# Kernel tuning notes

Hardware: AMD Instinct MI355X
Metric: run time of the kernel (lower is better)

The kernel has to match this reference:

```python
import jax, jax.numpy as jnp
import numpy as np

SEQ, BATCH, IN, HID = 512, 64, 512, 1024


def setup_inputs() -> dict:
    key = jax.random.key(0)
    k_x, k_wih, k_whh, k_bih, k_bhh = jax.random.split(key, 5)
    s = 1.0 / np.sqrt(HID)  # PyTorch GRU init: U(-1/sqrt(H), 1/sqrt(H))
    return {
        "x": jax.random.normal(k_x, (SEQ, BATCH, IN), dtype=jnp.float32),
        "W_ih": jax.random.uniform(k_wih, (3 * HID, IN), jnp.float32, -s, s),
        "W_hh": jax.random.uniform(k_whh, (3 * HID, HID), jnp.float32, -s, s),
        "b_ih": jax.random.uniform(k_bih, (3 * HID,), jnp.float32, -s, s),
        "b_hh": jax.random.uniform(k_bhh, (3 * HID,), jnp.float32, -s, s),
    }


def reference(x, W_ih, W_hh, b_ih, b_hh):
    """Single-layer GRU, PyTorch gate semantics, h0 = 0.
    r = sig(Wir x + bir + Whr h + bhr); z = sig(...);
    n = tanh(Win x + bin + r * (Whn h + bhn)); h' = (1-z)*n + z*h.
    Returns (outputs [S,B,H], hidden [1,B,H])."""
    H = W_hh.shape[1]
    # Precompute all input-side gate projections in one big GEMM: (S,B,3H)
    gates_x = jnp.einsum("sbi,gi->sbg", x, W_ih) + b_ih

    def step(h, gx):
        gh = h @ W_hh.T + b_hh  # (B, 3H)
        xr, xz, xn = jnp.split(gx, 3, axis=-1)
        hr, hz, hn = jnp.split(gh, 3, axis=-1)
        r = jax.nn.sigmoid(xr + hr)
        z = jax.nn.sigmoid(xz + hz)
        n = jnp.tanh(xn + r * hn)
        h_new = (1.0 - z) * n + z * h
        return h_new, h_new

    h0 = jnp.zeros((x.shape[1], H), dtype=x.dtype)
    h_last, ys = jax.lax.scan(step, h0, gates_x)
    return ys, h_last[None]  # match nn.GRU: (output, hidden[num_layers=1])
```

## Files before the change

kernel.cpp:

```cpp
#include <hip/hip_runtime.h>
#include <stdint.h>


#define SEQ    512
#define BATCH  64
#define IN_DIM 512
#define HID    1024
#define G3     3072
#define NBLK   256

typedef __bf16 bf16x8 __attribute__((ext_vector_type(8)));
typedef short  s16x8  __attribute__((ext_vector_type(8)));
typedef float  f32x4  __attribute__((ext_vector_type(4)));
typedef unsigned int u32x4 __attribute__((ext_vector_type(4)));

__device__ __forceinline__ float bf2f(unsigned int u) {
    union { unsigned int i; float f; } c; c.i = u << 16; return c.f;
}
__device__ __forceinline__ unsigned short f2bf(float f) {
    union { float f; unsigned int i; } c; c.f = f;
    unsigned int u = c.i;
    u += 0x7fffu + ((u >> 16) & 1u);
    return (unsigned short)(u >> 16);
}

__global__ void cvt_f32_bf16(const float* __restrict__ in,
                             unsigned short* __restrict__ out, int n) {
    int i = (blockIdx.x * 256 + threadIdx.x) * 4;
    if (i + 3 < n) {
        float4 v = *(const float4*)(in + i);
        ushort4 o;
        o.x = f2bf(v.x); o.y = f2bf(v.y); o.z = f2bf(v.z); o.w = f2bf(v.w);
        *(ushort4*)(out + i) = o;
    }
}

__global__ void init_state(unsigned int* __restrict__ h0,
                           unsigned int* __restrict__ h1,
                           unsigned int* __restrict__ flags) {
    int i = blockIdx.x * 256 + threadIdx.x;
    if (i < BATCH * HID) { h0[i] = 0u; h1[i] = 0u; }
    if (i < NBLK * 4)    flags[i] = 0u;
}

__global__ __launch_bounds__(256) void gx_gemm(
    const unsigned short* __restrict__ xb,
    const unsigned short* __restrict__ wb,
    const float* __restrict__ bih,
    unsigned short* __restrict__ gx) {
    const int lane = threadIdx.x & 63;
    const int wv   = threadIdx.x >> 6;
    const int r    = lane & 15;
    const int quad = lane >> 4;
    const int m0 = blockIdx.x * 128 + (wv & 1) * 64;
    const int n0 = blockIdx.y * 128 + (wv >> 1) * 64;

    f32x4 acc[4][4];
#pragma unroll
    for (int a = 0; a < 4; a++)
#pragma unroll
        for (int b = 0; b < 4; b++) acc[a][b] = (f32x4){0.f, 0.f, 0.f, 0.f};

    const unsigned short* ap[4];
    const unsigned short* bp[4];
#pragma unroll
    for (int mi = 0; mi < 4; mi++)
        ap[mi] = xb + (size_t)(m0 + mi * 16 + r) * IN_DIM + quad * 8;
#pragma unroll
    for (int ni = 0; ni < 4; ni++)
        bp[ni] = wb + (size_t)(n0 + ni * 16 + r) * IN_DIM + quad * 8;

#pragma unroll 4
    for (int kk = 0; kk < IN_DIM / 32; kk++) {
        bf16x8 af[4], bf_[4];
#pragma unroll
        for (int mi = 0; mi < 4; mi++)
            af[mi] = __builtin_bit_cast(bf16x8, *(const s16x8*)(ap[mi] + kk * 32));
#pragma unroll
        for (int ni = 0; ni < 4; ni++)
            bf_[ni] = __builtin_bit_cast(bf16x8, *(const s16x8*)(bp[ni] + kk * 32));
#pragma unroll
        for (int mi = 0; mi < 4; mi++)
#pragma unroll
            for (int ni = 0; ni < 4; ni++)
                acc[mi][ni] = __builtin_amdgcn_mfma_f32_16x16x32_bf16(
                    af[mi], bf_[ni], acc[mi][ni], 0, 0, 0);
    }

#pragma unroll
    for (int ni = 0; ni < 4; ni++) {
        const int col = n0 + ni * 16 + r;
        const float bias = bih[col];
#pragma unroll
        for (int mi = 0; mi < 4; mi++)
#pragma unroll
            for (int i = 0; i < 4; i++) {
                const int row = m0 + mi * 16 + quad * 4 + i;
                gx[(size_t)row * G3 + col] = f2bf(acc[mi][ni][i] + bias);
            }
    }
}

#define HL16(dst, OFF)                                                    \
    asm volatile("global_load_dwordx4 %0, %1, off offset:" OFF " sc0 sc1" \
                 : "=&v"(dst) : "v"(hbase))
#define SL4(dst, BASE)                                                    \
    asm volatile("global_load_dword %0, %1, off sc0 sc1"                  \
                 : "=&v"(dst) : "v"(BASE))

__global__ __launch_bounds__(256, 2) void gru_seq(
    const unsigned short* __restrict__ whb,
    const float* __restrict__ bhh,
    const unsigned short* __restrict__ gxb,
    unsigned int* __restrict__ h0,
    unsigned int* __restrict__ h1,
    unsigned int* __restrict__ flags,
    float* __restrict__ out) {
    const int lane = threadIdx.x & 63;
    const int wv   = threadIdx.x >> 6;
    const int r    = lane & 15;
    const int quad = lane >> 4;
    const int cg   = blockIdx.x & 63;
    const int bh   = blockIdx.x >> 6;
    const int J0   = cg * 16;
    const int R0   = bh * 16;
    const int k0   = wv * 256;

    __shared__ float red[4][3][4][64];
    __shared__ int dead;
    if (threadIdx.x == 0) dead = 0;
    __syncthreads();

    const unsigned short* wrp = whb + (size_t)(J0 + r) * HID + k0 + quad * 8;
    const unsigned short* wzp = wrp + (size_t)HID * HID;
    const unsigned short* wnp = wrp + (size_t)2 * HID * HID;
    u32x4 wRv[8], wZv[8], wNv[8];
#pragma unroll
    for (int kk = 0; kk < 8; kk++) {
        wRv[kk] = *(const u32x4*)(wrp + kk * 32);
        wZv[kk] = *(const u32x4*)(wzp + kk * 32);
        wNv[kk] = *(const u32x4*)(wnp + kk * 32);
    }
#pragma unroll
    for (int kk = 0; kk < 8; kk++) {
        asm volatile("" : "+v"(wRv[kk]), "+v"(wZv[kk]), "+v"(wNv[kk]));
    }
    const float bhr = bhh[J0 + r];
    const float bhz = bhh[HID + J0 + r];
    const float bhn = bhh[2 * HID + J0 + r];

    const int    arow = R0 + r;
    const int    erow = R0 + quad * 4 + wv;
    const size_t hidx = (size_t)erow * HID + J0 + r;
    const unsigned int* fbase = flags + (size_t)(bh * 256 + lane * 4);
    const int myflag = bh * 256 + cg * 4;

    const unsigned short* gpr = gxb + (size_t)erow * G3 + J0 + r;
    float xr = bf2f(gpr[0]);
    float xz = bf2f(gpr[HID]);
    float xn = bf2f(gpr[2 * HID]);
    unsigned int hwpack = 0u;

#pragma unroll 1
    for (int t = 0; t < SEQ; t++) {
        const unsigned int* cur = (t & 1) ? h1 : h0;
        unsigned int*       nxt = (t & 1) ? h0 : h1;

        const unsigned int* hbase = cur + (size_t)arow * HID + k0 + quad * 8;
        u32x4 q[16];
        HL16(q[0],  "0");    HL16(q[1],  "16");
        HL16(q[2],  "128");  HL16(q[3],  "144");
        HL16(q[4],  "256");  HL16(q[5],  "272");
        HL16(q[6],  "384");  HL16(q[7],  "400");
        HL16(q[8],  "512");  HL16(q[9],  "528");
        HL16(q[10], "640");  HL16(q[11], "656");
        HL16(q[12], "768");  HL16(q[13], "784");
        HL16(q[14], "896");  HL16(q[15], "912");
        asm volatile("s_waitcnt vmcnt(0)" ::: "memory");
        __builtin_amdgcn_sched_barrier(0);

        f32x4 aR = {0.f, 0.f, 0.f, 0.f};
        f32x4 aZ = {0.f, 0.f, 0.f, 0.f};
        f32x4 aN = {0.f, 0.f, 0.f, 0.f};
#pragma unroll
        for (int kk = 0; kk < 8; kk++) {
            const u32x4 qa = q[2 * kk];
            const u32x4 qb = q[2 * kk + 1];
            u32x4 ahw, alw;
            ahw[0] = __builtin_amdgcn_perm(qa[1], qa[0], 0x07060302u);
            alw[0] = __builtin_amdgcn_perm(qa[1], qa[0], 0x05040100u);
            ahw[1] = __builtin_amdgcn_perm(qa[3], qa[2], 0x07060302u);
            alw[1] = __builtin_amdgcn_perm(qa[3], qa[2], 0x05040100u);
            ahw[2] = __builtin_amdgcn_perm(qb[1], qb[0], 0x07060302u);
            alw[2] = __builtin_amdgcn_perm(qb[1], qb[0], 0x05040100u);
            ahw[3] = __builtin_amdgcn_perm(qb[3], qb[2], 0x07060302u);
            alw[3] = __builtin_amdgcn_perm(qb[3], qb[2], 0x05040100u);
            bf16x8 ah = __builtin_bit_cast(bf16x8, ahw);
            bf16x8 al = __builtin_bit_cast(bf16x8, alw);
            bf16x8 fr = __builtin_bit_cast(bf16x8, wRv[kk]);
            bf16x8 fz = __builtin_bit_cast(bf16x8, wZv[kk]);
            bf16x8 fn = __builtin_bit_cast(bf16x8, wNv[kk]);
            aR = __builtin_amdgcn_mfma_f32_16x16x32_bf16(ah, fr, aR, 0, 0, 0);
            aZ = __builtin_amdgcn_mfma_f32_16x16x32_bf16(ah, fz, aZ, 0, 0, 0);
            aN = __builtin_amdgcn_mfma_f32_16x16x32_bf16(ah, fn, aN, 0, 0, 0);
            aR = __builtin_amdgcn_mfma_f32_16x16x32_bf16(al, fr, aR, 0, 0, 0);
            aZ = __builtin_amdgcn_mfma_f32_16x16x32_bf16(al, fz, aZ, 0, 0, 0);
            aN = __builtin_amdgcn_mfma_f32_16x16x32_bf16(al, fn, aN, 0, 0, 0);
        }

#pragma unroll
        for (int i = 0; i < 4; i++) {
            red[wv][0][i][lane] = aR[i];
            red[wv][1][i][lane] = aZ[i];
            red[wv][2][i][lane] = aN[i];
        }
        __syncthreads();

        const float sR = red[0][0][wv][lane] + red[1][0][wv][lane]
                       + red[2][0][wv][lane] + red[3][0][wv][lane];
        const float sZ = red[0][1][wv][lane] + red[1][1][wv][lane]
                       + red[2][1][wv][lane] + red[3][1][wv][lane];
        const float sN = red[0][2][wv][lane] + red[1][2][wv][lane]
                       + red[2][2][wv][lane] + red[3][2][wv][lane];
        const float hold = bf2f(hwpack >> 16) + bf2f(hwpack & 0xffffu);
        const float rg = 1.f / (1.f + __expf(-(xr + sR + bhr)));
        const float zg = 1.f / (1.f + __expf(-(xz + sZ + bhz)));
        const float e2 = __expf(2.f * (xn + rg * (sN + bhn)));
        const float ng = 1.f - 2.f / (e2 + 1.f);
        const float hn = (1.f - zg) * ng + zg * hold;
        const unsigned int uhi = f2bf(hn);
        const unsigned int ulo = f2bf(hn - bf2f(uhi));
        hwpack = (uhi << 16) | ulo;
        {
            unsigned int oldswp = __hip_atomic_exchange(
                nxt + hidx, hwpack, __ATOMIC_RELAXED, __HIP_MEMORY_SCOPE_AGENT);
            asm volatile("" :: "v"(oldswp));
        }

        if (t != SEQ - 1) {
            __syncthreads();
            if (threadIdx.x == 0)
                __hip_atomic_store(flags + myflag, (unsigned int)(t + 1),
                                   __ATOMIC_RELAXED, __HIP_MEMORY_SCOPE_AGENT);
            out[(size_t)t * (BATCH * HID) + hidx] = hn;
            gpr += BATCH * G3;
            xr = bf2f(gpr[0]);
            xz = bf2f(gpr[HID]);
            xn = bf2f(gpr[2 * HID]);
            if (wv == 0 && !dead) {
                const unsigned int tgt = (unsigned int)(t + 1);
                int guard = 0;
                for (;;) {
                    unsigned int f0;
                    SL4(f0, fbase);
                    asm volatile("s_waitcnt vmcnt(0)" ::: "memory");
                    __builtin_amdgcn_sched_barrier(0);
                    if (__all(f0 >= tgt)) break;
                    if (++guard > (1 << 17)) {
                        if (lane == 0) dead = 1;
                        break;
                    }
                    __builtin_amdgcn_s_sleep(1);
                }
            }
            __syncthreads();
        } else {
            out[(size_t)t * (BATCH * HID) + hidx] = hn;
            out[(size_t)SEQ * (BATCH * HID) + hidx] = hn;
        }
    }
}

extern "C" void kernel_launch(void* const* d_in, const int* in_sizes, int n_in,
                              void* d_out, int out_size, void* d_ws, size_t ws_size,
                              hipStream_t stream) {
    const float* x   = (const float*)d_in[0];
    const float* Wih = (const float*)d_in[1];
    const float* Whh = (const float*)d_in[2];
    const float* bih = (const float*)d_in[3];
    const float* bhh = (const float*)d_in[4];
    float* out = (float*)d_out;

    char* ws = (char*)d_ws;
    size_t off = 0;
    auto alloc = [&](size_t bytes) {
        char* p = ws + off;
        off += (bytes + 255) & ~(size_t)255;
        return p;
    };
    unsigned int*   flags = (unsigned int*)alloc((size_t)NBLK * 16);
    unsigned int*   h0    = (unsigned int*)alloc((size_t)BATCH * HID * 4);
    unsigned int*   h1    = (unsigned int*)alloc((size_t)BATCH * HID * 4);
    unsigned short* xb    = (unsigned short*)alloc((size_t)SEQ * BATCH * IN_DIM * 2);
    unsigned short* wihb  = (unsigned short*)alloc((size_t)G3 * IN_DIM * 2);
    unsigned short* whhb  = (unsigned short*)alloc((size_t)G3 * HID * 2);
    unsigned short* gxb   = (unsigned short*)alloc((size_t)SEQ * BATCH * G3 * 2);
    (void)ws_size; (void)in_sizes; (void)n_in; (void)out_size;

    init_state<<<(BATCH * HID + 255) / 256, 256, 0, stream>>>(h0, h1, flags);
    cvt_f32_bf16<<<(SEQ * BATCH * IN_DIM / 4) / 256, 256, 0, stream>>>(
        x, xb, SEQ * BATCH * IN_DIM);
    cvt_f32_bf16<<<(G3 * IN_DIM / 4) / 256, 256, 0, stream>>>(Wih, wihb, G3 * IN_DIM);
    cvt_f32_bf16<<<(G3 * HID / 4) / 256, 256, 0, stream>>>(Whh, whhb, G3 * HID);
    gx_gemm<<<dim3(SEQ * BATCH / 128, G3 / 128), 256, 0, stream>>>(
        xb, wihb, bih, gxb);

    gru_seq<<<dim3(NBLK), dim3(256), 0, stream>>>(
        whhb, bhh, gxb, h0, h1, flags, out);
}
```

Measured before the change: 3.124 ms.

## Store packed hidden state in output buffer and drop register-resident weights

The recurrent kernel no longer keeps separate h0/h1 ping-pong buffers. Each step writes its packed bf16 hi/lo state straight into the output tensor, and the next step reads the previous timestep's slice from there. A new fix_out pass then converts the whole packed output back to fp32. The kernel also stops preloading W_hh fragments into registers and reloads them from global memory inside every step. The separate fp32 output store and the explicit sc0/sc1 cache-bypassing loads are removed. This trades a redundant store for weight reloads on the latency-critical serial path plus an extra full pass over the output.

```diff
diff --git a/kernel.cpp b/kernel.cpp
--- a/kernel.cpp
+++ b/kernel.cpp
@@ -8,6 +8,7 @@
 #define HID    1024
 #define G3     3072
 #define NBLK   256
+#define BH     (BATCH * HID)
 
 typedef __bf16 bf16x8 __attribute__((ext_vector_type(8)));
 typedef short  s16x8  __attribute__((ext_vector_type(8)));
@@ -35,12 +36,23 @@
     }
 }
 
-__global__ void init_state(unsigned int* __restrict__ h0,
-                           unsigned int* __restrict__ h1,
-                           unsigned int* __restrict__ flags) {
+__global__ void init_state(unsigned int* __restrict__ flags) {
     int i = blockIdx.x * 256 + threadIdx.x;
-    if (i < BATCH * HID) { h0[i] = 0u; h1[i] = 0u; }
-    if (i < NBLK * 4)    flags[i] = 0u;
+    if (i < NBLK * 4) flags[i] = 0u;
+}
+
+__global__ __launch_bounds__(256) void fix_out(unsigned int* __restrict__ o,
+                                               int n) {
+    int i = (blockIdx.x * 256 + threadIdx.x) * 4;
+    if (i + 3 < n) {
+        u32x4 u = *(const u32x4*)(o + i);
+        float f0 = bf2f(u[0] >> 16) + bf2f(u[0] & 0xffffu);
+        float f1 = bf2f(u[1] >> 16) + bf2f(u[1] & 0xffffu);
+        float f2 = bf2f(u[2] >> 16) + bf2f(u[2] & 0xffffu);
+        float f3 = bf2f(u[3] >> 16) + bf2f(u[3] & 0xffffu);
+        float4 v = {f0, f1, f2, f3};
+        *(float4*)(o + i) = __builtin_bit_cast(float4, v);
+    }
 }
 
 __global__ __launch_bounds__(256) void gx_gemm(
@@ -101,9 +113,6 @@
     }
 }
 
-#define HL16(dst, OFF)                                                    \
-    asm volatile("global_load_dwordx4 %0, %1, off offset:" OFF " sc0 sc1" \
-                 : "=&v"(dst) : "v"(hbase))
 #define SL4(dst, BASE)                                                    \
     asm volatile("global_load_dword %0, %1, off sc0 sc1"                  \
                  : "=&v"(dst) : "v"(BASE))
@@ -112,10 +121,8 @@
     const unsigned short* __restrict__ whb,
     const float* __restrict__ bhh,
     const unsigned short* __restrict__ gxb,
-    unsigned int* __restrict__ h0,
-    unsigned int* __restrict__ h1,
     unsigned int* __restrict__ flags,
-    float* __restrict__ out) {
+    unsigned int* __restrict__ outw) {
     const int lane = threadIdx.x & 63;
     const int wv   = threadIdx.x >> 6;
     const int r    = lane & 15;
@@ -134,17 +141,6 @@
     const unsigned short* wrp = whb + (size_t)(J0 + r) * HID + k0 + quad * 8;
     const unsigned short* wzp = wrp + (size_t)HID * HID;
     const unsigned short* wnp = wrp + (size_t)2 * HID * HID;
-    u32x4 wRv[8], wZv[8], wNv[8];
-#pragma unroll
-    for (int kk = 0; kk < 8; kk++) {
-        wRv[kk] = *(const u32x4*)(wrp + kk * 32);
-        wZv[kk] = *(const u32x4*)(wzp + kk * 32);
-        wNv[kk] = *(const u32x4*)(wnp + kk * 32);
-    }
-#pragma unroll
-    for (int kk = 0; kk < 8; kk++) {
-        asm volatile("" : "+v"(wRv[kk]), "+v"(wZv[kk]), "+v"(wNv[kk]));
-    }
     const float bhr = bhh[J0 + r];
     const float bhz = bhh[HID + J0 + r];
     const float bhn = bhh[2 * HID + J0 + r];
@@ -152,6 +148,7 @@
     const int    arow = R0 + r;
     const int    erow = R0 + quad * 4 + wv;
     const size_t hidx = (size_t)erow * HID + J0 + r;
+    const size_t aoff = (size_t)arow * HID + k0 + quad * 8;
     const unsigned int* fbase = flags + (size_t)(bh * 256 + lane * 4);
     const int myflag = bh * 256 + cg * 4;
 
@@ -163,49 +160,43 @@
 
 #pragma unroll 1
     for (int t = 0; t < SEQ; t++) {
-        const unsigned int* cur = (t & 1) ? h1 : h0;
-        unsigned int*       nxt = (t & 1) ? h0 : h1;
-
-        const unsigned int* hbase = cur + (size_t)arow * HID + k0 + quad * 8;
-        u32x4 q[16];
-        HL16(q[0],  "0");    HL16(q[1],  "16");
-        HL16(q[2],  "128");  HL16(q[3],  "144");
-        HL16(q[4],  "256");  HL16(q[5],  "272");
-        HL16(q[6],  "384");  HL16(q[7],  "400");
-        HL16(q[8],  "512");  HL16(q[9],  "528");
-        HL16(q[10], "640");  HL16(q[11], "656");
-        HL16(q[12], "768");  HL16(q[13], "784");
-        HL16(q[14], "896");  HL16(q[15], "912");
-        asm volatile("s_waitcnt vmcnt(0)" ::: "memory");
-        __builtin_amdgcn_sched_barrier(0);
-
         f32x4 aR = {0.f, 0.f, 0.f, 0.f};
         f32x4 aZ = {0.f, 0.f, 0.f, 0.f};
         f32x4 aN = {0.f, 0.f, 0.f, 0.f};
-#pragma unroll
-        for (int kk = 0; kk < 8; kk++) {
-            const u32x4 qa = q[2 * kk];
-            const u32x4 qb = q[2 * kk + 1];
-            u32x4 ahw, alw;
-            ahw[0] = __builtin_amdgcn_perm(qa[1], qa[0], 0x07060302u);
-            alw[0] = __builtin_amdgcn_perm(qa[1], qa[0], 0x05040100u);
-            ahw[1] = __builtin_amdgcn_perm(qa[3], qa[2], 0x07060302u);
-            alw[1] = __builtin_amdgcn_perm(qa[3], qa[2], 0x05040100u);
-            ahw[2] = __builtin_amdgcn_perm(qb[1], qb[0], 0x07060302u);
-            alw[2] = __builtin_amdgcn_perm(qb[1], qb[0], 0x05040100u);
-            ahw[3] = __builtin_amdgcn_perm(qb[3], qb[2], 0x07060302u);
-            alw[3] = __builtin_amdgcn_perm(qb[3], qb[2], 0x05040100u);
-            bf16x8 ah = __builtin_bit_cast(bf16x8, ahw);
-            bf16x8 al = __builtin_bit_cast(bf16x8, alw);
-            bf16x8 fr = __builtin_bit_cast(bf16x8, wRv[kk]);
-            bf16x8 fz = __builtin_bit_cast(bf16x8, wZv[kk]);
-            bf16x8 fn = __builtin_bit_cast(bf16x8, wNv[kk]);
-            aR = __builtin_amdgcn_mfma_f32_16x16x32_bf16(ah, fr, aR, 0, 0, 0);
-            aZ = __builtin_amdgcn_mfma_f32_16x16x32_bf16(ah, fz, aZ, 0, 0, 0);
-            aN = __builtin_amdgcn_mfma_f32_16x16x32_bf16(ah, fn, aN, 0, 0, 0);
-            aR = __builtin_amdgcn_mfma_f32_16x16x32_bf16(al, fr, aR, 0, 0, 0);
-            aZ = __builtin_amdgcn_mfma_f32_16x16x32_bf16(al, fz, aZ, 0, 0, 0);
-            aN = __builtin_amdgcn_mfma_f32_16x16x32_bf16(al, fn, aN, 0, 0, 0);
+
+        if (t > 0) {
+            const unsigned int* hbase = outw + (size_t)(t - 1) * BH + aoff;
+            u32x4 q[16];
+#pragma unroll
+            for (int kk = 0; kk < 8; kk++) {
+                q[2 * kk]     = *(const u32x4*)(hbase + kk * 32);
+                q[2 * kk + 1] = *(const u32x4*)(hbase + kk * 32 + 4);
+            }
+#pragma unroll
+            for (int kk = 0; kk < 8; kk++) {
+                const u32x4 qa = q[2 * kk];
+                const u32x4 qb = q[2 * kk + 1];
+                u32x4 ahw, alw;
+                ahw[0] = __builtin_amdgcn_perm(qa[1], qa[0], 0x07060302u);
+                alw[0] = __builtin_amdgcn_perm(qa[1], qa[0], 0x05040100u);
+                ahw[1] = __builtin_amdgcn_perm(qa[3], qa[2], 0x07060302u);
+                alw[1] = __builtin_amdgcn_perm(qa[3], qa[2], 0x05040100u);
+                ahw[2] = __builtin_amdgcn_perm(qb[1], qb[0], 0x07060302u);
+                alw[2] = __builtin_amdgcn_perm(qb[1], qb[0], 0x05040100u);
+                ahw[3] = __builtin_amdgcn_perm(qb[3], qb[2], 0x07060302u);
+                alw[3] = __builtin_amdgcn_perm(qb[3], qb[2], 0x05040100u);
+                bf16x8 ah = __builtin_bit_cast(bf16x8, ahw);
+                bf16x8 al = __builtin_bit_cast(bf16x8, alw);
+                bf16x8 fr = __builtin_bit_cast(bf16x8, *(const s16x8*)(wrp + kk * 32));
+                bf16x8 fz = __builtin_bit_cast(bf16x8, *(const s16x8*)(wzp + kk * 32));
+                bf16x8 fn = __builtin_bit_cast(bf16x8, *(const s16x8*)(wnp + kk * 32));
+                aR = __builtin_amdgcn_mfma_f32_16x16x32_bf16(ah, fr, aR, 0, 0, 0);
+                aZ = __builtin_amdgcn_mfma_f32_16x16x32_bf16(ah, fz, aZ, 0, 0, 0);
+                aN = __builtin_amdgcn_mfma_f32_16x16x32_bf16(ah, fn, aN, 0, 0, 0);
+                aR = __builtin_amdgcn_mfma_f32_16x16x32_bf16(al, fr, aR, 0, 0, 0);
+                aZ = __builtin_amdgcn_mfma_f32_16x16x32_bf16(al, fz, aZ, 0, 0, 0);
+                aN = __builtin_amdgcn_mfma_f32_16x16x32_bf16(al, fn, aN, 0, 0, 0);
+            }
         }
 
 #pragma unroll
@@ -233,7 +224,8 @@
         hwpack = (uhi << 16) | ulo;
         {
             unsigned int oldswp = __hip_atomic_exchange(
-                nxt + hidx, hwpack, __ATOMIC_RELAXED, __HIP_MEMORY_SCOPE_AGENT);
+                outw + (size_t)t * BH + hidx, hwpack,
+                __ATOMIC_RELAXED, __HIP_MEMORY_SCOPE_AGENT);
             asm volatile("" :: "v"(oldswp));
         }
 
@@ -242,7 +234,6 @@
             if (threadIdx.x == 0)
                 __hip_atomic_store(flags + myflag, (unsigned int)(t + 1),
                                    __ATOMIC_RELAXED, __HIP_MEMORY_SCOPE_AGENT);
-            out[(size_t)t * (BATCH * HID) + hidx] = hn;
             gpr += BATCH * G3;
             xr = bf2f(gpr[0]);
             xz = bf2f(gpr[HID]);
@@ -265,8 +256,7 @@
             }
             __syncthreads();
         } else {
-            out[(size_t)t * (BATCH * HID) + hidx] = hn;
-            out[(size_t)SEQ * (BATCH * HID) + hidx] = hn;
+            outw[(size_t)SEQ * BH + hidx] = hwpack;
         }
     }
 }
@@ -289,15 +279,13 @@
         return p;
     };
     unsigned int*   flags = (unsigned int*)alloc((size_t)NBLK * 16);
-    unsigned int*   h0    = (unsigned int*)alloc((size_t)BATCH * HID * 4);
-    unsigned int*   h1    = (unsigned int*)alloc((size_t)BATCH * HID * 4);
     unsigned short* xb    = (unsigned short*)alloc((size_t)SEQ * BATCH * IN_DIM * 2);
     unsigned short* wihb  = (unsigned short*)alloc((size_t)G3 * IN_DIM * 2);
     unsigned short* whhb  = (unsigned short*)alloc((size_t)G3 * HID * 2);
     unsigned short* gxb   = (unsigned short*)alloc((size_t)SEQ * BATCH * G3 * 2);
     (void)ws_size; (void)in_sizes; (void)n_in; (void)out_size;
 
-    init_state<<<(BATCH * HID + 255) / 256, 256, 0, stream>>>(h0, h1, flags);
+    init_state<<<4, 256, 0, stream>>>(flags);
     cvt_f32_bf16<<<(SEQ * BATCH * IN_DIM / 4) / 256, 256, 0, stream>>>(
         x, xb, SEQ * BATCH * IN_DIM);
     cvt_f32_bf16<<<(G3 * IN_DIM / 4) / 256, 256, 0, stream>>>(Wih, wihb, G3 * IN_DIM);
@@ -306,5 +294,9 @@
         xb, wihb, bih, gxb);
 
     gru_seq<<<dim3(NBLK), dim3(256), 0, stream>>>(
-        whhb, bhh, gxb, h0, h1, flags, out);
-}
+        whhb, bhh, gxb, flags, (unsigned int*)out);
+
+    const int n_out = (SEQ + 1) * BH;
+    fix_out<<<(n_out / 4 + 255) / 256, 256, 0, stream>>>(
+        (unsigned int*)out, n_out);
+}
```

Result: slower. 4.826 ms (+54.5%).
